# Kernel optimization log

Measured on AMD Instinct MI355X. Metric: run time of the kernel, lower is better.

## Reference

```python
import jax, jax.numpy as jnp
import numpy as np

N_NODES = 100000
N_EDGES = 1600000
IN_DIM, FEAT_DIM, HID_DIM, OUT_DIM = 256, 128, 128, 128


def _glorot(key, shape):
    lim = float(np.sqrt(6.0 / (shape[0] + shape[1])))
    return jax.random.uniform(key, shape, jnp.float32, -lim, lim)


def setup_inputs() -> dict:
    key = jax.random.key(0)
    ks = jax.random.split(key, 6)
    x = jax.random.normal(ks[0], (N_NODES, IN_DIM), jnp.float32)
    edge_index = jax.random.randint(ks[1], (2, N_EDGES), 0, N_NODES, dtype=jnp.int64)
    return {
        "x": x,
        "edge_index": edge_index,
        "Wp": _glorot(ks[2], (IN_DIM, FEAT_DIM)),
        "bp": jnp.zeros((FEAT_DIM,), jnp.float32),
        "W1": _glorot(ks[3], (FEAT_DIM, HID_DIM)),
        "b1": jnp.zeros((HID_DIM,), jnp.float32),
        "W2": _glorot(ks[4], (HID_DIM, OUT_DIM)),
        "b2": jnp.zeros((OUT_DIM,), jnp.float32),
    }


def _gcn_conv(h, W, b, src, dst, norm, deg_inv, n):
    # PyG GCNConv: linear first, symmetric-normalized aggregation (with
    # self-loops), bias after aggregation. Self-loop term = z_i / deg_i.
    z = h @ W                                   # [N, out]
    msg = (norm[src] * norm[dst])[:, None] * z[src]  # [E, out]
    agg = jax.ops.segment_sum(msg, dst, num_segments=n)
    return agg + z * deg_inv[:, None] + b


def reference(x, edge_index, Wp, bp, W1, b1, W2, b2):
    src, dst = edge_index[0], edge_index[1]
    n = x.shape[0]
    # degrees on A + I (self-loop adds 1)
    deg = jax.ops.segment_sum(jnp.ones(src.shape[0], x.dtype), dst, num_segments=n) + 1.0
    norm = jax.lax.rsqrt(deg)
    deg_inv = 1.0 / deg
    h = x @ Wp + bp                              # feature_pre linear
    h = jax.nn.relu(_gcn_conv(h, W1, b1, src, dst, norm, deg_inv, n))
    # dropout is identity in eval mode; layer_num=2 -> no hidden convs
    return _gcn_conv(h, W2, b2, src, dst, norm, deg_inv, n)
```

## Files before the change

### kernel.cpp

```cpp
#include <hip/hip_runtime.h>
#include <cstdint>
#include <cstddef>

#define N_NODES 100000
#define N_EDGES 1600000

constexpr int NPB = 512;
constexpr int NBUCK = (N_NODES + NPB - 1) / NPB;
constexpr int EPB = 8192;
constexpr int NCHUNK = (N_EDGES + EPB - 1) / EPB;

typedef _Float16 half8 __attribute__((ext_vector_type(8)));
typedef _Float16 half4v __attribute__((ext_vector_type(4)));
typedef _Float16 half2v __attribute__((ext_vector_type(2)));
typedef float f32x4 __attribute__((ext_vector_type(4)));

__global__ __launch_bounds__(256) void b1_hist(const int* __restrict__ dst,
                                               int* __restrict__ bbc) {
    __shared__ int hist[NBUCK];
    int t = threadIdx.x;
    if (t < NBUCK) hist[t] = 0;
    __syncthreads();
    int base = blockIdx.x * EPB;
#pragma unroll
    for (int i = 0; i < EPB / 256; ++i) {
        int e = base + i * 256 + t;
        if (e < N_EDGES) atomicAdd(&hist[dst[e] >> 9], 1);
    }
    __syncthreads();
    if (t < NBUCK) bbc[t * NCHUNK + blockIdx.x] = hist[t];
}

__global__ void b_scan(int* __restrict__ bbc, int* __restrict__ bucketOff,
                       int* __restrict__ rowStart) {
    __shared__ int tot[NBUCK];
    int t = threadIdx.x;
    if (t < NBUCK) {
        int run = 0;
        for (int blk = 0; blk < NCHUNK; ++blk) {
            int idx = t * NCHUNK + blk;
            int c = bbc[idx];
            bbc[idx] = run;
            run += c;
        }
        tot[t] = run;
    }
    __syncthreads();
    if (t == 0) {
        int acc = 0;
        for (int b = 0; b < NBUCK; ++b) {
            bucketOff[b] = acc;
            acc += tot[b];
        }
        bucketOff[NBUCK] = acc;
        rowStart[N_NODES] = acc;
    }
}

__global__ __launch_bounds__(256) void b2_scatter(const int* __restrict__ src,
                                                  const int* __restrict__ dst,
                                                  const int* __restrict__ bbc,
                                                  const int* __restrict__ bucketOff,
                                                  int* __restrict__ staged) {
    __shared__ int cnt[NBUCK];
    __shared__ int base[NBUCK];
    int t = threadIdx.x;
    if (t < NBUCK) {
        cnt[t] = 0;
        base[t] = bucketOff[t] + bbc[t * NCHUNK + blockIdx.x];
    }
    __syncthreads();
    int ebase = blockIdx.x * EPB;
#pragma unroll
    for (int i = 0; i < EPB / 256; ++i) {
        int e = ebase + i * 256 + t;
        if (e < N_EDGES) {
            int d = dst[e];
            int b = d >> 9;
            int r = atomicAdd(&cnt[b], 1);
            staged[base[b] + r] = ((d & 511) << 17) | src[e];
        }
    }
}

__global__ __launch_bounds__(256) void b3_sort(const int* __restrict__ staged,
                                               const int* __restrict__ bucketOff,
                                               int* __restrict__ rowStart,
                                               float* __restrict__ normv,
                                               int* __restrict__ colIdx) {
    __shared__ int hist[NPB];
    __shared__ int sc0[NPB], sc1[NPB];
    __shared__ int cursor[NPB];
    int t = threadIdx.x;
    int b = blockIdx.x;
    int e0 = bucketOff[b], e1 = bucketOff[b + 1];
    int ne = e1 - e0;
    int node0 = b * NPB;
    int nn = min(NPB, N_NODES - node0);

    for (int j = t; j < NPB; j += 256) hist[j] = 0;
    __syncthreads();
    for (int idx = t; idx < ne; idx += 256)
        atomicAdd(&hist[staged[e0 + idx] >> 17], 1);
    __syncthreads();
    for (int j = t; j < NPB; j += 256) sc0[j] = hist[j];
    __syncthreads();
    int* s = sc0;
    int* d = sc1;
    for (int off = 1; off < NPB; off <<= 1) {
        for (int j = t; j < NPB; j += 256) d[j] = s[j] + (j >= off ? s[j - off] : 0);
        __syncthreads();
        int* tmp = s; s = d; d = tmp;
    }
    for (int j = t; j < NPB; j += 256) {
        int excl = s[j] - hist[j];
        cursor[j] = excl;
        if (j < nn) {
            rowStart[node0 + j] = e0 + excl;
            normv[node0 + j] = (float)(1.0 / sqrt((double)(hist[j] + 1)));
        }
    }
    __syncthreads();
    for (int idx = t; idx < ne; idx += 256) {
        int v = staged[e0 + idx];
        int dl = v >> 17;
        int sn = v & 0x1FFFF;
        int r = atomicAdd(&cursor[dl], 1);
        colIdx[e0 + r] = sn;
    }
}

__global__ void wc_kernel(const float* __restrict__ Wp, const float* __restrict__ bp,
                          const float* __restrict__ W1, float* __restrict__ Wc,
                          float* __restrict__ bc) {
    int r = blockIdx.x;
    int cc = threadIdx.x;
    float acc = 0.f;
    if (r < 256) {
        for (int k = 0; k < 128; ++k) acc = fmaf(Wp[r * 128 + k], W1[k * 128 + cc], acc);
        Wc[r * 128 + cc] = acc;
    } else {
        for (int k = 0; k < 128; ++k) acc = fmaf(bp[k], W1[k * 128 + cc], acc);
        bc[cc] = acc;
    }
}

__global__ void tsplit_kernel(const float* __restrict__ W, _Float16* __restrict__ Oh,
                              _Float16* __restrict__ Ol, int K) {
    int id = blockIdx.x * 256 + threadIdx.x;
    if (id >= K * 128) return;
    int n = id / K;
    int k = id - n * K;
    float v = W[k * 128 + n];
    _Float16 h = (_Float16)v;
    Oh[id] = h;
    Ol[id] = (_Float16)(v - (float)h);
}

template <bool AF16>
__global__ __launch_bounds__(256) void mfma_gemm(const float* __restrict__ Af,
                                                 const _Float16* __restrict__ Ah,
                                                 const _Float16* __restrict__ Bth,
                                                 const _Float16* __restrict__ Btl,
                                                 const float* __restrict__ bias,
                                                 const float* __restrict__ scale,
                                                 float* __restrict__ Cf,
                                                 _Float16* __restrict__ Ch,
                                                 int M, int K) {
    __shared__ _Float16 sAh[128 * 40];
    __shared__ _Float16 sAl[AF16 ? 8 : 128 * 40];
    __shared__ _Float16 sBh[128 * 40];
    __shared__ _Float16 sBl[128 * 40];
    const int t = threadIdx.x;
    const int w = t >> 6;
    const int lane = t & 63;
    const int q = lane >> 4;
    const int mr = lane & 15;
    const int row0 = blockIdx.x * 128;

    f32x4 acc[2][8];
#pragma unroll
    for (int mt = 0; mt < 2; ++mt)
#pragma unroll
        for (int nt = 0; nt < 8; ++nt) acc[mt][nt] = (f32x4){0.f, 0.f, 0.f, 0.f};

    for (int k0 = 0; k0 < K; k0 += 32) {
        if constexpr (AF16) {
#pragma unroll
            for (int i = 0; i < 2; ++i) {
                int id = t + i * 256;
                int r = id >> 2;
                int c8 = (id & 3) * 8;
                half8 v = {0, 0, 0, 0, 0, 0, 0, 0};
                if (row0 + r < M) v = *(const half8*)(Ah + (size_t)(row0 + r) * K + k0 + c8);
                *(half8*)&sAh[r * 40 + c8] = v;
            }
        } else {
#pragma unroll
            for (int i = 0; i < 4; ++i) {
                int id = t + i * 256;
                int r = id >> 3;
                int c4 = (id & 7) * 4;
                float4 v = make_float4(0.f, 0.f, 0.f, 0.f);
                if (row0 + r < M) v = *(const float4*)(Af + (size_t)(row0 + r) * K + k0 + c4);
                half4v hh, ll;
                hh[0] = (_Float16)v.x; ll[0] = (_Float16)(v.x - (float)hh[0]);
                hh[1] = (_Float16)v.y; ll[1] = (_Float16)(v.y - (float)hh[1]);
                hh[2] = (_Float16)v.z; ll[2] = (_Float16)(v.z - (float)hh[2]);
                hh[3] = (_Float16)v.w; ll[3] = (_Float16)(v.w - (float)hh[3]);
                *(half4v*)&sAh[r * 40 + c4] = hh;
                *(half4v*)&sAl[r * 40 + c4] = ll;
            }
        }
#pragma unroll
        for (int i = 0; i < 2; ++i) {
            int id = t + i * 256;
            int n = id >> 2;
            int c8 = (id & 3) * 8;
            *(half8*)&sBh[n * 40 + c8] = *(const half8*)(Bth + (size_t)n * K + k0 + c8);
            *(half8*)&sBl[n * 40 + c8] = *(const half8*)(Btl + (size_t)n * K + k0 + c8);
        }
        __syncthreads();

        half8 ah[2], al[2], bh[8], bl[8];
#pragma unroll
        for (int mt = 0; mt < 2; ++mt) {
            int m = w * 32 + mt * 16 + mr;
            ah[mt] = *(half8*)&sAh[m * 40 + q * 8];
            if constexpr (!AF16) al[mt] = *(half8*)&sAl[m * 40 + q * 8];
        }
#pragma unroll
        for (int nt = 0; nt < 8; ++nt) {
            int n = nt * 16 + mr;
            bh[nt] = *(half8*)&sBh[n * 40 + q * 8];
            bl[nt] = *(half8*)&sBl[n * 40 + q * 8];
        }
#pragma unroll
        for (int mt = 0; mt < 2; ++mt)
#pragma unroll
            for (int nt = 0; nt < 8; ++nt) {
                acc[mt][nt] = __builtin_amdgcn_mfma_f32_16x16x32_f16(ah[mt], bh[nt], acc[mt][nt], 0, 0, 0);
                acc[mt][nt] = __builtin_amdgcn_mfma_f32_16x16x32_f16(ah[mt], bl[nt], acc[mt][nt], 0, 0, 0);
                if constexpr (!AF16)
                    acc[mt][nt] = __builtin_amdgcn_mfma_f32_16x16x32_f16(al[mt], bh[nt], acc[mt][nt], 0, 0, 0);
            }
        __syncthreads();
    }

#pragma unroll
    for (int mt = 0; mt < 2; ++mt) {
#pragma unroll
        for (int r = 0; r < 4; ++r) {
            int row = row0 + w * 32 + mt * 16 + q * 4 + r;
            if (row >= M) continue;
            float sc = scale[row];
#pragma unroll
            for (int nt = 0; nt < 8; ++nt) {
                int col = nt * 16 + mr;
                float bv = bias ? bias[col] : 0.f;
                float val = (acc[mt][nt][r] + bv) * sc;
                if (Ch) Ch[(size_t)row * 128 + col] = (_Float16)val;
                else    Cf[(size_t)row * 128 + col] = val;
            }
        }
    }
}

__global__ __launch_bounds__(256) void agg_kernel(const _Float16* __restrict__ zs,
                                                  const int* __restrict__ rowStart,
                                                  const int* __restrict__ colIdx,
                                                  const float* __restrict__ normv,
                                                  const float* __restrict__ bias,
                                                  float* __restrict__ outF,
                                                  _Float16* __restrict__ outH,
                                                  int doRelu) {
    int wid = (blockIdx.x * 256 + threadIdx.x) >> 6;
    int lane = threadIdx.x & 63;
    if (wid >= N_NODES) return;
    int s0 = rowStart[wid];
    int s1 = rowStart[wid + 1];
    const int c = lane * 2;
    const _Float16* zc = zs + c;

    float2 a0 = make_float2(0.f, 0.f), a1 = a0, a2 = a0, a3 = a0;
    int e = s0;
    for (; e + 8 <= s1; e += 8) {
        int i0 = colIdx[e + 0], i1 = colIdx[e + 1], i2 = colIdx[e + 2], i3 = colIdx[e + 3];
        int i4 = colIdx[e + 4], i5 = colIdx[e + 5], i6 = colIdx[e + 6], i7 = colIdx[e + 7];
        half2v v0 = *(const half2v*)(zc + (size_t)i0 * 128);
        half2v v1 = *(const half2v*)(zc + (size_t)i1 * 128);
        half2v v2 = *(const half2v*)(zc + (size_t)i2 * 128);
        half2v v3 = *(const half2v*)(zc + (size_t)i3 * 128);
        half2v v4 = *(const half2v*)(zc + (size_t)i4 * 128);
        half2v v5 = *(const half2v*)(zc + (size_t)i5 * 128);
        half2v v6 = *(const half2v*)(zc + (size_t)i6 * 128);
        half2v v7 = *(const half2v*)(zc + (size_t)i7 * 128);
        a0.x += (float)v0[0] + (float)v4[0]; a0.y += (float)v0[1] + (float)v4[1];
        a1.x += (float)v1[0] + (float)v5[0]; a1.y += (float)v1[1] + (float)v5[1];
        a2.x += (float)v2[0] + (float)v6[0]; a2.y += (float)v2[1] + (float)v6[1];
        a3.x += (float)v3[0] + (float)v7[0]; a3.y += (float)v3[1] + (float)v7[1];
    }
    if (e + 4 <= s1) {
        int i0 = colIdx[e + 0], i1 = colIdx[e + 1], i2 = colIdx[e + 2], i3 = colIdx[e + 3];
        half2v v0 = *(const half2v*)(zc + (size_t)i0 * 128);
        half2v v1 = *(const half2v*)(zc + (size_t)i1 * 128);
        half2v v2 = *(const half2v*)(zc + (size_t)i2 * 128);
        half2v v3 = *(const half2v*)(zc + (size_t)i3 * 128);
        a0.x += (float)v0[0]; a0.y += (float)v0[1];
        a1.x += (float)v1[0]; a1.y += (float)v1[1];
        a2.x += (float)v2[0]; a2.y += (float)v2[1];
        a3.x += (float)v3[0]; a3.y += (float)v3[1];
        e += 4;
    }
    for (; e < s1; ++e) {
        int i0 = colIdx[e];
        half2v v0 = *(const half2v*)(zc + (size_t)i0 * 128);
        a0.x += (float)v0[0]; a0.y += (float)v0[1];
    }

    half2v self = *(const half2v*)(zc + (size_t)wid * 128);
    float sx = (a0.x + a1.x) + (a2.x + a3.x) + (float)self[0];
    float sy = (a0.y + a1.y) + (a2.y + a3.y) + (float)self[1];
    float nd = normv[wid];
    float2 bv = *(const float2*)(bias + c);
    float ox = fmaf(nd, sx, bv.x);
    float oy = fmaf(nd, sy, bv.y);
    if (doRelu) {
        ox = fmaxf(ox, 0.f);
        oy = fmaxf(oy, 0.f);
    }
    if (outH) {
        half2v o;
        o[0] = (_Float16)ox;
        o[1] = (_Float16)oy;
        *(half2v*)(outH + (size_t)wid * 128 + c) = o;
    } else {
        *(float2*)(outF + (size_t)wid * 128 + c) = make_float2(ox, oy);
    }
}

extern "C" void kernel_launch(void* const* d_in, const int* in_sizes, int n_in,
                              void* d_out, int out_size, void* d_ws, size_t ws_size,
                              hipStream_t stream) {
    const float* x  = (const float*)d_in[0];
    const int* ei   = (const int*)d_in[1];
    const float* Wp = (const float*)d_in[2];
    const float* bp = (const float*)d_in[3];
    const float* W1 = (const float*)d_in[4];
    const float* b1 = (const float*)d_in[5];
    const float* W2 = (const float*)d_in[6];
    const float* b2 = (const float*)d_in[7];
    float* out = (float*)d_out;

    const int* srcIdx = ei;
    const int* dstIdx = ei + N_EDGES;

    size_t off = 0;
    auto alloc = [&](size_t bytes) -> void* {
        void* p = (char*)d_ws + off;
        off += (bytes + 511) & ~(size_t)511;
        return p;
    };
    int* rowStart   = (int*)alloc((size_t)(N_NODES + 1) * 4);
    int* colIdx     = (int*)alloc((size_t)N_EDGES * 4);
    int* staged     = (int*)alloc((size_t)N_EDGES * 4);
    int* bbc        = (int*)alloc((size_t)NBUCK * NCHUNK * 4);
    int* bucketOff  = (int*)alloc((size_t)(NBUCK + 1) * 4);
    float* normv    = (float*)alloc((size_t)N_NODES * 4);
    float* Wc       = (float*)alloc((size_t)256 * 128 * 4);
    float* bc       = (float*)alloc((size_t)128 * 4);
    _Float16* Wcth  = (_Float16*)alloc((size_t)128 * 256 * 2);
    _Float16* Wctl  = (_Float16*)alloc((size_t)128 * 256 * 2);
    _Float16* W2th  = (_Float16*)alloc((size_t)128 * 128 * 2);
    _Float16* W2tl  = (_Float16*)alloc((size_t)128 * 128 * 2);
    _Float16* zA    = (_Float16*)alloc((size_t)N_NODES * 128 * 2);
    _Float16* zB    = (_Float16*)alloc((size_t)N_NODES * 128 * 2);

    const int GB = (N_NODES + 127) / 128;
    const int AB = (N_NODES + 3) / 4;

    b1_hist<<<NCHUNK, 256, 0, stream>>>(dstIdx, bbc);
    b_scan<<<1, 256, 0, stream>>>(bbc, bucketOff, rowStart);
    b2_scatter<<<NCHUNK, 256, 0, stream>>>(srcIdx, dstIdx, bbc, bucketOff, staged);
    b3_sort<<<NBUCK, 256, 0, stream>>>(staged, bucketOff, rowStart, normv, colIdx);

    wc_kernel<<<257, 128, 0, stream>>>(Wp, bp, W1, Wc, bc);
    tsplit_kernel<<<(256 * 128 + 255) / 256, 256, 0, stream>>>(Wc, Wcth, Wctl, 256);
    tsplit_kernel<<<(128 * 128 + 255) / 256, 256, 0, stream>>>(W2, W2th, W2tl, 128);

    mfma_gemm<false><<<GB, 256, 0, stream>>>(x, nullptr, Wcth, Wctl, bc, normv,
                                             nullptr, zA, N_NODES, 256);
    agg_kernel<<<AB, 256, 0, stream>>>(zA, rowStart, colIdx, normv, b1, nullptr, zB, 1);
    mfma_gemm<true><<<GB, 256, 0, stream>>>(nullptr, zB, W2th, W2tl, nullptr, normv,
                                            nullptr, zA, N_NODES, 128);
    agg_kernel<<<AB, 256, 0, stream>>>(zA, rowStart, colIdx, normv, b2, out, nullptr, 0);
}
```

Measured before the change: 483.9 us.

## Load MFMA operands directly from global memory, dropping LDS staging and barriers

The MFMA GEMM no longer stages A and B tiles through shared memory with __syncthreads. Each wave now loads its own A fragments, and all B fragments, straight from global into registers in MFMA layout. Out-of-range rows are clamped to row 0 rather than zero-filled. This removes LDS traffic and barrier stalls, but each wave re-reads B from global/L2 and A loads become less coalesced per lane.

```diff
diff --git a/kernel.cpp b/kernel.cpp
--- a/kernel.cpp
+++ b/kernel.cpp
@@ -11,7 +11,6 @@
 constexpr int NCHUNK = (N_EDGES + EPB - 1) / EPB;
 
 typedef _Float16 half8 __attribute__((ext_vector_type(8)));
-typedef _Float16 half4v __attribute__((ext_vector_type(4)));
 typedef _Float16 half2v __attribute__((ext_vector_type(2)));
 typedef float f32x4 __attribute__((ext_vector_type(4)));
 
@@ -167,16 +166,15 @@
                                                  float* __restrict__ Cf,
                                                  _Float16* __restrict__ Ch,
                                                  int M, int K) {
-    __shared__ _Float16 sAh[128 * 40];
-    __shared__ _Float16 sAl[AF16 ? 8 : 128 * 40];
-    __shared__ _Float16 sBh[128 * 40];
-    __shared__ _Float16 sBl[128 * 40];
     const int t = threadIdx.x;
     const int w = t >> 6;
     const int lane = t & 63;
     const int q = lane >> 4;
     const int mr = lane & 15;
-    const int row0 = blockIdx.x * 128;
+    const int row0 = blockIdx.x * 128 + w * 32;
+
+    int ar0 = row0 + mr;        if (ar0 >= M) ar0 = 0;
+    int ar1 = row0 + 16 + mr;   if (ar1 >= M) ar1 = 0;
 
     f32x4 acc[2][8];
 #pragma unroll
@@ -185,73 +183,47 @@
         for (int nt = 0; nt < 8; ++nt) acc[mt][nt] = (f32x4){0.f, 0.f, 0.f, 0.f};
 
     for (int k0 = 0; k0 < K; k0 += 32) {
+        const int kf = k0 + q * 8;
+        half8 ah[2], al[2];
         if constexpr (AF16) {
-#pragma unroll
-            for (int i = 0; i < 2; ++i) {
-                int id = t + i * 256;
-                int r = id >> 2;
-                int c8 = (id & 3) * 8;
-                half8 v = {0, 0, 0, 0, 0, 0, 0, 0};
-                if (row0 + r < M) v = *(const half8*)(Ah + (size_t)(row0 + r) * K + k0 + c8);
-                *(half8*)&sAh[r * 40 + c8] = v;
+            ah[0] = *(const half8*)(Ah + (size_t)ar0 * K + kf);
+            ah[1] = *(const half8*)(Ah + (size_t)ar1 * K + kf);
+        } else {
+#pragma unroll
+            for (int mt = 0; mt < 2; ++mt) {
+                int row = mt ? ar1 : ar0;
+                const float* ap = Af + (size_t)row * K + kf;
+                float4 v0 = *(const float4*)ap;
+                float4 v1 = *(const float4*)(ap + 4);
+                float av[8] = {v0.x, v0.y, v0.z, v0.w, v1.x, v1.y, v1.z, v1.w};
+#pragma unroll
+                for (int j = 0; j < 8; ++j) {
+                    _Float16 h = (_Float16)av[j];
+                    ah[mt][j] = h;
+                    al[mt][j] = (_Float16)(av[j] - (float)h);
+                }
             }
-        } else {
-#pragma unroll
-            for (int i = 0; i < 4; ++i) {
-                int id = t + i * 256;
-                int r = id >> 3;
-                int c4 = (id & 7) * 4;
-                float4 v = make_float4(0.f, 0.f, 0.f, 0.f);
-                if (row0 + r < M) v = *(const float4*)(Af + (size_t)(row0 + r) * K + k0 + c4);
-                half4v hh, ll;
-                hh[0] = (_Float16)v.x; ll[0] = (_Float16)(v.x - (float)hh[0]);
-                hh[1] = (_Float16)v.y; ll[1] = (_Float16)(v.y - (float)hh[1]);
-                hh[2] = (_Float16)v.z; ll[2] = (_Float16)(v.z - (float)hh[2]);
-                hh[3] = (_Float16)v.w; ll[3] = (_Float16)(v.w - (float)hh[3]);
-                *(half4v*)&sAh[r * 40 + c4] = hh;
-                *(half4v*)&sAl[r * 40 + c4] = ll;
-            }
-        }
-#pragma unroll
-        for (int i = 0; i < 2; ++i) {
-            int id = t + i * 256;
-            int n = id >> 2;
-            int c8 = (id & 3) * 8;
-            *(half8*)&sBh[n * 40 + c8] = *(const half8*)(Bth + (size_t)n * K + k0 + c8);
-            *(half8*)&sBl[n * 40 + c8] = *(const half8*)(Btl + (size_t)n * K + k0 + c8);
-        }
-        __syncthreads();
-
-        half8 ah[2], al[2], bh[8], bl[8];
-#pragma unroll
-        for (int mt = 0; mt < 2; ++mt) {
-            int m = w * 32 + mt * 16 + mr;
-            ah[mt] = *(half8*)&sAh[m * 40 + q * 8];
-            if constexpr (!AF16) al[mt] = *(half8*)&sAl[m * 40 + q * 8];
         }
 #pragma unroll
         for (int nt = 0; nt < 8; ++nt) {
             int n = nt * 16 + mr;
-            bh[nt] = *(half8*)&sBh[n * 40 + q * 8];
-            bl[nt] = *(half8*)&sBl[n * 40 + q * 8];
-        }
-#pragma unroll
-        for (int mt = 0; mt < 2; ++mt)
-#pragma unroll
-            for (int nt = 0; nt < 8; ++nt) {
-                acc[mt][nt] = __builtin_amdgcn_mfma_f32_16x16x32_f16(ah[mt], bh[nt], acc[mt][nt], 0, 0, 0);
-                acc[mt][nt] = __builtin_amdgcn_mfma_f32_16x16x32_f16(ah[mt], bl[nt], acc[mt][nt], 0, 0, 0);
+            half8 bh = *(const half8*)(Bth + (size_t)n * K + kf);
+            half8 bl = *(const half8*)(Btl + (size_t)n * K + kf);
+#pragma unroll
+            for (int mt = 0; mt < 2; ++mt) {
+                acc[mt][nt] = __builtin_amdgcn_mfma_f32_16x16x32_f16(ah[mt], bh, acc[mt][nt], 0, 0, 0);
+                acc[mt][nt] = __builtin_amdgcn_mfma_f32_16x16x32_f16(ah[mt], bl, acc[mt][nt], 0, 0, 0);
                 if constexpr (!AF16)
-                    acc[mt][nt] = __builtin_amdgcn_mfma_f32_16x16x32_f16(al[mt], bh[nt], acc[mt][nt], 0, 0, 0);
+                    acc[mt][nt] = __builtin_amdgcn_mfma_f32_16x16x32_f16(al[mt], bh, acc[mt][nt], 0, 0, 0);
             }
-        __syncthreads();
+        }
     }
 
 #pragma unroll
     for (int mt = 0; mt < 2; ++mt) {
 #pragma unroll
         for (int r = 0; r < 4; ++r) {
-            int row = row0 + w * 32 + mt * 16 + q * 4 + r;
+            int row = row0 + mt * 16 + q * 4 + r;
             if (row >= M) continue;
             float sc = scale[row];
 #pragma unroll
```

Result: slower. 516.5 us (+6.7%).
